# Kernel tuning notes

Hardware: AMD Instinct MI355X
Metric: run time of the kernel (lower is better)

Reference implementation:

```python
import jax, jax.numpy as jnp
import numpy as np

H = 48        # num attention heads
D = 128       # head dim
KV = 1        # multi-query: single KV head


def setup_inputs() -> dict:
    key = jax.random.key(0)
    ks = jax.random.split(key, 5)
    B, S, HID = 1, 2048, 6144
    QKV_OUT = HID + 2 * KV * D  # 6400
    scale = 0.02
    return {
        "x": jax.random.normal(ks[0], (B, S, HID), jnp.float32),
        "wqkv": jax.random.normal(ks[1], (QKV_OUT, HID), jnp.float32) * scale,
        "bqkv": jax.random.normal(ks[2], (QKV_OUT,), jnp.float32) * scale,
        "wo": jax.random.normal(ks[3], (HID, HID), jnp.float32) * scale,
        "bo": jax.random.normal(ks[4], (HID,), jnp.float32) * scale,
    }


def reference(x, wqkv, bqkv, wo, bo):
    B, S, HID = x.shape
    # fused QKV projection (c_attn), bias=True
    qkv = jnp.einsum('bsh,oh->bso', x, wqkv) + bqkv          # [B,S,6400]
    q = qkv[..., :HID].reshape(B, S, H, D)                    # [B,S,H,D]
    k = qkv[..., HID:HID + KV * D].reshape(B, S, D)           # [B,S,D] (single KV head)
    v = qkv[..., HID + KV * D:].reshape(B, S, D)              # [B,S,D]

    # multi-query causal attention: all H query heads attend to the one KV head
    scores = jnp.einsum('bqhd,bkd->bhqk', q, k) * (1.0 / np.sqrt(D).astype(np.float32))
    causal = jnp.tril(jnp.ones((S, S), dtype=bool))
    scores = jnp.where(causal[None, None], scores, jnp.finfo(scores.dtype).min)
    probs = jax.nn.softmax(scores, axis=-1)                   # [B,H,S,S]
    attn = jnp.einsum('bhqk,bkd->bqhd', probs, v)             # [B,S,H,D]
    attn = attn.reshape(B, S, H * D)                          # [B,S,HID]

    # output projection (c_proj), bias added (bias_pre_add semantics are TP-only)
    return jnp.einsum('bsh,oh->bso', attn, wo) + bo
```

## Files before the change

kernel.cpp:

```cpp
#include <hip/hip_runtime.h>
#include <hip/hip_bf16.h>
#include <cstdint>
#include <cstddef>

#define SEQ  2048
#define HID_ 6144
#define NKV  6400
#define NH_  48
#define HD_  128

typedef unsigned short u16;
typedef __bf16 bf16x8 __attribute__((ext_vector_type(8)));
typedef float  f32x4  __attribute__((ext_vector_type(4)));
typedef unsigned short us8 __attribute__((ext_vector_type(8)));

__device__ __forceinline__ void async_ld16(const void* g, void* l) {
  __builtin_amdgcn_global_load_lds(
      (const __attribute__((address_space(1))) unsigned int*)g,
      (__attribute__((address_space(3))) unsigned int*)l, 16, 0, 0);
}

__device__ __forceinline__ u16 f2b(float f) {
  __hip_bfloat16 h = __float2bfloat16(f);
  return *reinterpret_cast<u16*>(&h);
}

__global__ void cvt_f32_bf16(const float* __restrict__ in, u16* __restrict__ out,
                             long n8) {
  const long i = (long)blockIdx.x * blockDim.x + threadIdx.x;
  if (i >= n8) return;
  const long o = i * 8;
  const float4 f0 = *(const float4*)(in + o);
  const float4 f1 = *(const float4*)(in + o + 4);
  us8 v;
  v[0] = f2b(f0.x); v[1] = f2b(f0.y); v[2] = f2b(f0.z); v[3] = f2b(f0.w);
  v[4] = f2b(f1.x); v[5] = f2b(f1.y); v[6] = f2b(f1.z); v[7] = f2b(f1.w);
  *(us8*)(out + o) = v;
}

template <int N, int K, typename OT>
__global__ __launch_bounds__(256, 2)
void gemm_bt_bias(const u16* __restrict__ A, const u16* __restrict__ B,
                  const float* __restrict__ bias, OT* __restrict__ C) {
  __shared__ u16 As[128 * 32];
  __shared__ u16 Bs[128 * 32];
  const int tid  = threadIdx.x;
  const int lane = tid & 63, wave = tid >> 6;
  const int l15  = lane & 15, quad = lane >> 4;
  const int wm = wave >> 1, wn = wave & 1;
  const int m0 = blockIdx.y * 128, n0 = blockIdx.x * 128;

  f32x4 acc[4][4];
#pragma unroll
  for (int i = 0; i < 4; ++i)
#pragma unroll
    for (int j = 0; j < 4; ++j) acc[i][j] = f32x4{0.f, 0.f, 0.f, 0.f};

  const int rowA0 = tid >> 2, col8 = (tid & 3) * 8;
  const u16* gA = A + (size_t)(m0 + rowA0) * K + col8;
  const u16* gB = B + (size_t)(n0 + rowA0) * K + col8;
  u16* lA = As + tid * 8;
  u16* lB = Bs + tid * 8;

  for (int k0 = 0; k0 < K; k0 += 32) {
    async_ld16(gA + k0, lA);
    async_ld16(gA + (size_t)64 * K + k0, lA + 256 * 8);
    async_ld16(gB + k0, lB);
    async_ld16(gB + (size_t)64 * K + k0, lB + 256 * 8);
    __syncthreads();

    const u16* aBase = As + (wm * 64 + l15) * 32 + quad * 8;
    const u16* bBase = Bs + (wn * 64 + l15) * 32 + quad * 8;
    bf16x8 af[4], bfr[4];
#pragma unroll
    for (int i = 0; i < 4; ++i) {
      af[i]  = *(const bf16x8*)(aBase + i * 16 * 32);
      bfr[i] = *(const bf16x8*)(bBase + i * 16 * 32);
    }
#pragma unroll
    for (int i = 0; i < 4; ++i)
#pragma unroll
      for (int j = 0; j < 4; ++j)
        acc[i][j] = __builtin_amdgcn_mfma_f32_16x16x32_bf16(af[i], bfr[j], acc[i][j], 0, 0, 0);
    __syncthreads();
  }

#pragma unroll
  for (int j = 0; j < 4; ++j) {
    const int n = n0 + wn * 64 + j * 16 + l15;
    const float bv = bias[n];
#pragma unroll
    for (int i = 0; i < 4; ++i) {
      const int mrow = m0 + wm * 64 + i * 16 + quad * 4;
#pragma unroll
      for (int r = 0; r < 4; ++r) {
        const float v = acc[i][j][r] + bv;
        if constexpr (sizeof(OT) == 2)
          C[(size_t)(mrow + r) * N + n] = (OT)f2b(v);
        else
          C[(size_t)(mrow + r) * N + n] = (OT)v;
      }
    }
  }
}

__global__ __launch_bounds__(256, 2)
void mqa_flash(const u16* __restrict__ qkv, u16* __restrict__ attn) {
  __shared__ u16 Ks[4 * 64 * 32];
  __shared__ u16 Vt[128 * 72];
  __shared__ u16 Ps[4 * 16 * 72];
  const int tid  = threadIdx.x;
  const int lane = tid & 63, wave = tid >> 6;
  const int l15  = lane & 15, quad = lane >> 4;
  const int h = blockIdx.y, qb = blockIdx.x;
  const int q0 = qb * 64;
  const float scale = 0.088388347648318447f;

  bf16x8 qf[4];
  {
    const u16* qp = qkv + (size_t)(q0 + wave * 16 + l15) * NKV + h * HD_ + quad * 8;
#pragma unroll
    for (int kc = 0; kc < 4; ++kc) qf[kc] = *(const bf16x8*)(qp + kc * 32);
  }

  f32x4 oacc[8];
#pragma unroll
  for (int nd = 0; nd < 8; ++nd) oacc[nd] = f32x4{0.f, 0.f, 0.f, 0.f};
  float mrun[4], lrun[4];
#pragma unroll
  for (int r = 0; r < 4; ++r) { mrun[r] = -1e30f; lrun[r] = 0.f; }

  const int kv2 = lane & 31;
  const int dg  = wave * 2 + (lane >> 5);

  for (int t = 0; t <= qb; ++t) {
    const int kv0 = t * 64;
#pragma unroll
    for (int r = 0; r < 4; ++r) {
      const int c = r * 256 + tid;
      const int kc = c >> 8, rr = (c >> 2) & 63, c8 = (c & 3) * 8;
      const u16* gp = qkv + (size_t)(kv0 + rr) * NKV + HID_ + kc * 32 + c8;
      async_ld16(gp, (void*)(Ks + c * 8));
    }
    {
      const u16* gp0 = qkv + (size_t)(kv0 + kv2 * 2) * NKV + HID_ + HD_ + dg * 16;
      const u16* gp1 = gp0 + NKV;
      us8 a0 = *(const us8*)gp0;
      us8 a1 = *(const us8*)(gp0 + 8);
      us8 b0 = *(const us8*)gp1;
      us8 b1 = *(const us8*)(gp1 + 8);
#pragma unroll
      for (int i = 0; i < 8; ++i) {
        unsigned v0 = (unsigned)a0[i] | ((unsigned)b0[i] << 16);
        unsigned v1 = (unsigned)a1[i] | ((unsigned)b1[i] << 16);
        *(unsigned*)(Vt + (dg * 16 + i) * 72 + kv2 * 2) = v0;
        *(unsigned*)(Vt + (dg * 16 + 8 + i) * 72 + kv2 * 2) = v1;
      }
    }
    __syncthreads();

    f32x4 s[4];
#pragma unroll
    for (int nt = 0; nt < 4; ++nt) {
      f32x4 c4 = f32x4{0.f, 0.f, 0.f, 0.f};
#pragma unroll
      for (int kc = 0; kc < 4; ++kc) {
        bf16x8 kf = *(const bf16x8*)(Ks + kc * 2048 + (nt * 16 + l15) * 32 + quad * 8);
        c4 = __builtin_amdgcn_mfma_f32_16x16x32_bf16(qf[kc], kf, c4, 0, 0, 0);
      }
      s[nt] = c4;
    }

    float mt[4] = {-1e30f, -1e30f, -1e30f, -1e30f};
#pragma unroll
    for (int nt = 0; nt < 4; ++nt) {
      const int kvg = kv0 + nt * 16 + l15;
#pragma unroll
      for (int r = 0; r < 4; ++r) {
        const int qg = q0 + wave * 16 + quad * 4 + r;
        float v = s[nt][r] * scale;
        v = (kvg <= qg) ? v : -1e30f;
        s[nt][r] = v;
        mt[r] = fmaxf(mt[r], v);
      }
    }
#pragma unroll
    for (int off = 1; off < 16; off <<= 1)
#pragma unroll
      for (int r = 0; r < 4; ++r) mt[r] = fmaxf(mt[r], __shfl_xor(mt[r], off));

    float alpha[4], rsum[4];
#pragma unroll
    for (int r = 0; r < 4; ++r) {
      const float mnew = fmaxf(mrun[r], mt[r]);
      alpha[r] = __expf(mrun[r] - mnew);
      mrun[r] = mnew;
      rsum[r] = 0.f;
    }
    u16* pw = Ps + wave * (16 * 72);
#pragma unroll
    for (int nt = 0; nt < 4; ++nt)
#pragma unroll
      for (int r = 0; r < 4; ++r) {
        const float p = __expf(s[nt][r] - mrun[r]);
        rsum[r] += p;
        pw[(quad * 4 + r) * 72 + nt * 16 + l15] = f2b(p);
      }
#pragma unroll
    for (int off = 1; off < 16; off <<= 1)
#pragma unroll
      for (int r = 0; r < 4; ++r) rsum[r] += __shfl_xor(rsum[r], off);
#pragma unroll
    for (int r = 0; r < 4; ++r) lrun[r] = lrun[r] * alpha[r] + rsum[r];
#pragma unroll
    for (int nd = 0; nd < 8; ++nd)
#pragma unroll
      for (int r = 0; r < 4; ++r) oacc[nd][r] *= alpha[r];

#pragma unroll
    for (int kc2 = 0; kc2 < 2; ++kc2) {
      bf16x8 pf = *(const bf16x8*)(pw + l15 * 72 + kc2 * 32 + quad * 8);
#pragma unroll
      for (int nd = 0; nd < 8; ++nd) {
        bf16x8 vf = *(const bf16x8*)(Vt + (nd * 16 + l15) * 72 + kc2 * 32 + quad * 8);
        oacc[nd] = __builtin_amdgcn_mfma_f32_16x16x32_bf16(pf, vf, oacc[nd], 0, 0, 0);
      }
    }
    __syncthreads();
  }

#pragma unroll
  for (int r = 0; r < 4; ++r) {
    const int qg = q0 + wave * 16 + quad * 4 + r;
    const float inv = 1.f / lrun[r];
#pragma unroll
    for (int nd = 0; nd < 8; ++nd)
      attn[(size_t)qg * HID_ + h * HD_ + nd * 16 + l15] = f2b(oacc[nd][r] * inv);
  }
}

extern "C" void kernel_launch(void* const* d_in, const int* in_sizes, int n_in,
                              void* d_out, int out_size, void* d_ws, size_t ws_size,
                              hipStream_t stream) {
  const float* x    = (const float*)d_in[0];
  const float* wqkv = (const float*)d_in[1];
  const float* bqkv = (const float*)d_in[2];
  const float* wo   = (const float*)d_in[3];
  const float* bo   = (const float*)d_in[4];
  float* out = (float*)d_out;

  u16* xb     = (u16*)d_ws;
  u16* wqkvb  = xb + (size_t)SEQ * HID_;
  u16* wob    = wqkvb + (size_t)NKV * HID_;
  u16* qkvws  = wob + (size_t)HID_ * HID_;
  u16* attnws = qkvws + (size_t)SEQ * NKV;

  {
    const long n8x = (long)SEQ * HID_ / 8;
    cvt_f32_bf16<<<(n8x + 255) / 256, 256, 0, stream>>>(x, xb, n8x);
    const long n8q = (long)NKV * HID_ / 8;
    cvt_f32_bf16<<<(n8q + 255) / 256, 256, 0, stream>>>(wqkv, wqkvb, n8q);
    const long n8o = (long)HID_ * HID_ / 8;
    cvt_f32_bf16<<<(n8o + 255) / 256, 256, 0, stream>>>(wo, wob, n8o);
  }

  gemm_bt_bias<NKV, HID_, u16><<<dim3(NKV / 128, SEQ / 128), 256, 0, stream>>>(
      xb, wqkvb, bqkv, qkvws);
  mqa_flash<<<dim3(SEQ / 64, NH_), 256, 0, stream>>>(qkvws, attnws);
  gemm_bt_bias<HID_, HID_, float><<<dim3(HID_ / 128, SEQ / 128), 256, 0, stream>>>(
      attnws, wob, bo, out);
}
```

Measured before the change: 1.034 ms.

## Register-prefetch next KV tile, reverse causal block order, skip mask off-diagonal

The flash attention kernel now loads the next K/V tile from global memory into registers while the current tile is computed, with double-buffered register sets, replacing direct async-to-LDS loads. The grid is transposed so the heavy causal query blocks are scheduled first and the heads sharing a KV tile run together, which improves load balance and L2 reuse. The causal mask is applied only on the diagonal tile, and launch bounds are raised to 3 blocks per CU. The intent is to hide global load latency and reduce tail imbalance, at the cost of more registers, which could cause spills under the tighter occupancy bound.

```diff
diff --git a/kernel.cpp b/kernel.cpp
--- a/kernel.cpp
+++ b/kernel.cpp
@@ -104,7 +104,7 @@
   }
 }
 
-__global__ __launch_bounds__(256, 2)
+__global__ __launch_bounds__(256, 3)
 void mqa_flash(const u16* __restrict__ qkv, u16* __restrict__ attn) {
   __shared__ u16 Ks[4 * 64 * 32];
   __shared__ u16 Vt[128 * 72];
@@ -112,7 +112,8 @@
   const int tid  = threadIdx.x;
   const int lane = tid & 63, wave = tid >> 6;
   const int l15  = lane & 15, quad = lane >> 4;
-  const int h = blockIdx.y, qb = blockIdx.x;
+  const int h  = blockIdx.x;
+  const int qb = (int)gridDim.y - 1 - (int)blockIdx.y;
   const int q0 = qb * 64;
   const float scale = 0.088388347648318447f;
 
@@ -130,35 +131,37 @@
 #pragma unroll
   for (int r = 0; r < 4; ++r) { mrun[r] = -1e30f; lrun[r] = 0.f; }
 
+  const int krow = tid >> 2, kc8 = (tid & 3) * 8;
   const int kv2 = lane & 31;
   const int dg  = wave * 2 + (lane >> 5);
 
-  for (int t = 0; t <= qb; ++t) {
+  auto load_tile = [&](int t, us8* kr, us8* vr) {
     const int kv0 = t * 64;
-#pragma unroll
-    for (int r = 0; r < 4; ++r) {
-      const int c = r * 256 + tid;
-      const int kc = c >> 8, rr = (c >> 2) & 63, c8 = (c & 3) * 8;
-      const u16* gp = qkv + (size_t)(kv0 + rr) * NKV + HID_ + kc * 32 + c8;
-      async_ld16(gp, (void*)(Ks + c * 8));
-    }
-    {
-      const u16* gp0 = qkv + (size_t)(kv0 + kv2 * 2) * NKV + HID_ + HD_ + dg * 16;
-      const u16* gp1 = gp0 + NKV;
-      us8 a0 = *(const us8*)gp0;
-      us8 a1 = *(const us8*)(gp0 + 8);
-      us8 b0 = *(const us8*)gp1;
-      us8 b1 = *(const us8*)(gp1 + 8);
-#pragma unroll
-      for (int i = 0; i < 8; ++i) {
-        unsigned v0 = (unsigned)a0[i] | ((unsigned)b0[i] << 16);
-        unsigned v1 = (unsigned)a1[i] | ((unsigned)b1[i] << 16);
-        *(unsigned*)(Vt + (dg * 16 + i) * 72 + kv2 * 2) = v0;
-        *(unsigned*)(Vt + (dg * 16 + 8 + i) * 72 + kv2 * 2) = v1;
-      }
-    }
-    __syncthreads();
-
+    const u16* kp = qkv + (size_t)(kv0 + krow) * NKV + HID_ + kc8;
+#pragma unroll
+    for (int r = 0; r < 4; ++r) kr[r] = *(const us8*)(kp + r * 32);
+    const u16* vp = qkv + (size_t)(kv0 + kv2 * 2) * NKV + HID_ + HD_ + dg * 16;
+    vr[0] = *(const us8*)(vp);
+    vr[1] = *(const us8*)(vp + 8);
+    vr[2] = *(const us8*)(vp + NKV);
+    vr[3] = *(const us8*)(vp + NKV + 8);
+  };
+
+  auto stage_tile = [&](const us8* kr, const us8* vr) {
+    u16* kd = Ks + tid * 8;
+#pragma unroll
+    for (int r = 0; r < 4; ++r) *(us8*)(kd + r * 2048) = kr[r];
+#pragma unroll
+    for (int i = 0; i < 8; ++i) {
+      unsigned v0 = (unsigned)vr[0][i] | ((unsigned)vr[2][i] << 16);
+      unsigned v1 = (unsigned)vr[1][i] | ((unsigned)vr[3][i] << 16);
+      *(unsigned*)(Vt + (dg * 16 + i) * 72 + kv2 * 2) = v0;
+      *(unsigned*)(Vt + (dg * 16 + 8 + i) * 72 + kv2 * 2) = v1;
+    }
+  };
+
+  auto compute_tile = [&](int t) {
+    const int kv0 = t * 64;
     f32x4 s[4];
 #pragma unroll
     for (int nt = 0; nt < 4; ++nt) {
@@ -172,17 +175,28 @@
     }
 
     float mt[4] = {-1e30f, -1e30f, -1e30f, -1e30f};
-#pragma unroll
-    for (int nt = 0; nt < 4; ++nt) {
-      const int kvg = kv0 + nt * 16 + l15;
-#pragma unroll
-      for (int r = 0; r < 4; ++r) {
-        const int qg = q0 + wave * 16 + quad * 4 + r;
-        float v = s[nt][r] * scale;
-        v = (kvg <= qg) ? v : -1e30f;
-        s[nt][r] = v;
-        mt[r] = fmaxf(mt[r], v);
-      }
+    if (t == qb) {
+#pragma unroll
+      for (int nt = 0; nt < 4; ++nt) {
+        const int kvg = kv0 + nt * 16 + l15;
+#pragma unroll
+        for (int r = 0; r < 4; ++r) {
+          const int qg = q0 + wave * 16 + quad * 4 + r;
+          float v = s[nt][r] * scale;
+          v = (kvg <= qg) ? v : -1e30f;
+          s[nt][r] = v;
+          mt[r] = fmaxf(mt[r], v);
+        }
+      }
+    } else {
+#pragma unroll
+      for (int nt = 0; nt < 4; ++nt)
+#pragma unroll
+        for (int r = 0; r < 4; ++r) {
+          const float v = s[nt][r] * scale;
+          s[nt][r] = v;
+          mt[r] = fmaxf(mt[r], v);
+        }
     }
 #pragma unroll
     for (int off = 1; off < 16; off <<= 1)
@@ -226,6 +240,21 @@
         oacc[nd] = __builtin_amdgcn_mfma_f32_16x16x32_bf16(pf, vf, oacc[nd], 0, 0, 0);
       }
     }
+  };
+
+  us8 kA[4], vA[4], kB[4], vB[4];
+  load_tile(0, kA, vA);
+  for (int t = 0; t <= qb; ++t) {
+    const int tn = (t < qb) ? t + 1 : t;
+    if (!(t & 1)) {
+      stage_tile(kA, vA);
+      load_tile(tn, kB, vB);
+    } else {
+      stage_tile(kB, vB);
+      load_tile(tn, kA, vA);
+    }
+    __syncthreads();
+    compute_tile(t);
     __syncthreads();
   }
 
@@ -266,7 +295,7 @@
 
   gemm_bt_bias<NKV, HID_, u16><<<dim3(NKV / 128, SEQ / 128), 256, 0, stream>>>(
       xb, wqkvb, bqkv, qkvws);
-  mqa_flash<<<dim3(SEQ / 64, NH_), 256, 0, stream>>>(qkvws, attnws);
+  mqa_flash<<<dim3(NH_, SEQ / 64), 256, 0, stream>>>(qkvws, attnws);
   gemm_bt_bias<HID_, HID_, float><<<dim3(HID_ / 128, SEQ / 128), 256, 0, stream>>>(
       attnws, wob, bo, out);
 }
```

New measurement: 934.9 us. 9.6% less time.
